# Performance work log

Hardware: AMD Instinct MI355X
Metric: run time of the kernel (lower is better)

Reference implementation:

```python
import jax, jax.numpy as jnp
import numpy as np

N, C, L = 1024, 3, 6000
CONV_CH = [20, 32, 64, 20]
K = 3            # conv kernel size, padding (K-1)//2 = 1 -> SAME
POOL = 2
HID = 100
FLAT_DIM = (L // POOL**4 + 2 * C + 1) * CONV_CH[-1]  # (375 + 7) * 20 = 7640


def setup_inputs() -> dict:
    key = jax.random.key(0)
    ks = jax.random.split(key, 10)
    d = {"x": jax.random.normal(ks[0], (N, C, L), jnp.float32)}
    ins = [C] + CONV_CH[:-1]
    for i, (ic, oc) in enumerate(zip(ins, CONV_CH)):
        d[f"w{i}"] = jax.random.normal(ks[1 + i], (oc, ic, K), jnp.float32) * (1.0 / np.sqrt(ic * K))
        d[f"b{i}"] = jnp.zeros((oc,), jnp.float32)
    d["wc"] = jax.random.normal(ks[6], (CONV_CH[-1], C, 1), jnp.float32) * (1.0 / np.sqrt(C))
    d["bc"] = jnp.zeros((CONV_CH[-1],), jnp.float32)
    d["wl0"] = jax.random.normal(ks[7], (HID, FLAT_DIM), jnp.float32) * (1.0 / np.sqrt(FLAT_DIM))
    d["bl0"] = jnp.zeros((HID,), jnp.float32)
    d["wl1"] = jax.random.normal(ks[8], (2, HID), jnp.float32) * (1.0 / np.sqrt(HID))
    d["bl1"] = jnp.zeros((2,), jnp.float32)
    return d


def conv1d(x, w, b, pad):
    # x: (N, C_in, L), w: (C_out, C_in, K)
    out = jax.lax.conv_general_dilated(x, w, (1,), [(pad, pad)],
                                       dimension_numbers=('NCH', 'OIH', 'NCH'))
    return out + b[None, :, None]


def maxpool2(x):
    n, c, l = x.shape  # l always even here (6000 / 2^k)
    return x.reshape(n, c, l // 2, 2).max(-1)


def cov_eig_feats(x):
    # batched covariance as a single contraction (avoids the O(N*L*C*C) bmm intermediate)
    n, c, l = x.shape
    diff = x - x.mean(-1, keepdims=True)
    cov = jnp.einsum('ncl,ndl->ncd', diff, diff) / (l - 1)  # (N, C, C)
    # cov is symmetric PSD -> eigh (real); torch uses generic eig and keeps real parts
    vals, vecs = jnp.linalg.eigh(cov)
    vals = vals[..., None] / vals.max()          # global max over batch, like torch
    cov = cov / jnp.abs(cov).max()
    return jnp.concatenate([cov, vals, vecs], axis=-1)  # (N, C, 2C+1)


def reference(x, w0, b0, w1, b1, w2, b2, w3, b3, wc, bc, wl0, bl0, wl1, bl1):
    feats = jax.lax.stop_gradient(cov_eig_feats(x))  # torch branch is @no_grad
    h = x
    for w, b in ((w0, b0), (w1, b1), (w2, b2), (w3, b3)):
        h = maxpool2(jax.nn.relu(conv1d(h, w, b, (K - 1) // 2)))
    h = h.reshape(h.shape[0], -1)                    # (N, 20*375)
    h1 = jax.nn.relu(conv1d(feats, wc, bc, 0))       # (N, 20, 7)
    h1 = h1.reshape(h1.shape[0], -1)
    h = jnp.concatenate([h, h1], axis=1)             # (N, 7640)
    h = jax.nn.relu(h @ wl0.T + bl0)
    out = h @ wl1.T + bl1                            # (N, 2)
    return (out[:, :1], out[:, 1:])
```

## Files before the change

### kernel.cpp

```cpp
#include <hip/hip_runtime.h>
#include <hip/hip_fp16.h>
#include <math.h>

#define NBATCH 1024
#define LIN    6000
#define HCATW  7640
#define HID    100

#define TCH   54
#define NCHK  7

#define ASZ 3552
#define BSZ 4460

#define W0OFF 0
#define W1OFF 192
#define W2OFF 2112
#define W3OFF 8256
#define B0OFF 12352
#define B1OFF 12372
#define B2OFF 12404
#define B3OFF 12468
#define WREPSZ 12496

#define WL0HSZ (HID * (HCATW/2))

#define FCNS 8

typedef _Float16 v2h __attribute__((ext_vector_type(2)));

__device__ __forceinline__ float fdot2_f16(unsigned int a, unsigned int b, float c) {
#if __has_builtin(__builtin_amdgcn_fdot2)
    v2h ah, bh;
    __builtin_memcpy(&ah, &a, 4);
    __builtin_memcpy(&bh, &b, 4);
    return __builtin_amdgcn_fdot2(ah, bh, c, false);
#else
    float d;
    asm("v_dot2_f32_f16 %0, %1, %2, %3" : "=v"(d) : "v"(a), "v"(b), "v"(c));
    return d;
#endif
}

__device__ __forceinline__ __half2 u2h2(unsigned int u) {
    __half2 h; __builtin_memcpy(&h, &u, 4); return h;
}

__device__ __forceinline__ void pack_pk16g(int idx, int OC, int IC, int OCG,
                                           int OPG, int WSTR,
                                           const float* __restrict__ w,
                                           unsigned int* __restrict__ dst)
{
    if (idx >= OCG * IC * WSTR) return;
    int ocg = idx / (IC * WSTR);
    int r   = idx - ocg * (IC * WSTR);
    int ic  = r / WSTR, q = r - ic * WSTR;
    int o   = q / 3, k = q - o * 3;
    int oc  = ocg * OPG + o;
    unsigned int v = 0;
    if (o < OPG && oc < OC) {
        float wv = w[(oc * IC + ic) * 3 + k];
        unsigned int h = __half_as_ushort(__float2half(wv));
        v = h | (h << 16);
    }
    dst[idx] = v;
}

__global__ __launch_bounds__(256) void prep_kernel(
    const float* __restrict__ w0, const float* __restrict__ b0,
    const float* __restrict__ w1, const float* __restrict__ b1,
    const float* __restrict__ w2, const float* __restrict__ b2,
    const float* __restrict__ w3, const float* __restrict__ b3,
    const float* __restrict__ wl0,
    float* __restrict__ wrep, unsigned int* __restrict__ wl0h)
{
    int idx = blockIdx.x * 256 + threadIdx.x;
    if (idx < WL0HSZ) {
        float a = wl0[idx * 2], b = wl0[idx * 2 + 1];
        unsigned int lo = __half_as_ushort(__float2half(a));
        unsigned int hi = __half_as_ushort(__float2half(b));
        wl0h[idx] = lo | (hi << 16);
    }
    if (idx < 8192) {
        unsigned int* wu = (unsigned int*)wrep;
        pack_pk16g(idx, 20,  3, 4, 5, 16, w0, wu + W0OFF);
        pack_pk16g(idx, 32, 20, 4, 8, 24, w1, wu + W1OFF);
        pack_pk16g(idx, 64, 32, 8, 8, 24, w2, wu + W2OFF);
        pack_pk16g(idx, 20, 64, 4, 5, 16, w3, wu + W3OFF);
        if (idx < 20)            wrep[B0OFF + idx] = b0[idx];
        else if (idx < 52)  { int i = idx - 20;  wrep[B1OFF + i] = b1[i]; }
        else if (idx < 116) { int i = idx - 52;  wrep[B2OFF + i] = b2[i]; }
        else if (idx < 136) { int i = idx - 116; wrep[B3OFF + i] = b3[i]; }
    }
}

template<int IC, int OC, int OCG, int OPG, int WSTR, int JOUT, int LG, int JBLK,
         bool FINAL>
__device__ __forceinline__ void stage_eo(const float* __restrict__ in,
                                         float* __restrict__ out,
                                         float* __restrict__ outg,
                                         const float* __restrict__ wrep,
                                         const float* __restrict__ brep,
                                         int pbase, int o3, int wv, int lane,
                                         int zero)
{
    constexpr int PIN  = JOUT + 1;
    constexpr int NJT  = (JOUT + 64 * JBLK - 1) / (64 * JBLK);
    for (int task = wv; task < OCG * NJT; task += 8) {
        const int ocg = task / NJT;
        const int jt  = task - ocg * NJT;
        const int j0  = jt * (64 * JBLK) + lane;
        const float* bp = brep + ocg * OPG;
        __half2 ap[JBLK][OPG];
#pragma unroll
        for (int t = 0; t < JBLK; ++t)
#pragma unroll
            for (int o = 0; o < OPG; ++o) {
                __half hb = __float2half(bp[o]);
                ap[t][o] = __halves2half2(hb, hb);
            }
        const float* wbase = wrep + ocg * (IC * WSTR) + zero;
#pragma unroll 1
        for (int ic = 0; ic < IC; ++ic) {
            const float* wp = wbase + ic * WSTR;
            float wr[WSTR];
#pragma unroll
            for (int q = 0; q < WSTR / 4; ++q)
                *(float4*)&wr[q * 4] = *(const float4*)(wp + q * 4);
#pragma unroll
            for (int t = 0; t < JBLK; ++t) {
                const int jj = j0 + t * 64;
                const int jc = (jj < JOUT) ? jj : (JOUT - 1);
                const float* ipw = in + ic * PIN;
                uint2 pw;
                __builtin_memcpy(&pw, ipw + jc, 8);
                const unsigned int crossu = (pw.x >> 16) | (pw.y << 16);
#pragma unroll
                for (int o = 0; o < OPG; ++o) {
                    __half2 a = ap[t][o];
                    a = __hfma2(u2h2(pw.x),   u2h2(__float_as_uint(wr[o*3+0])), a);
                    a = __hfma2(u2h2(crossu), u2h2(__float_as_uint(wr[o*3+1])), a);
                    a = __hfma2(u2h2(pw.y),   u2h2(__float_as_uint(wr[o*3+2])), a);
                    ap[t][o] = a;
                }
            }
        }

#pragma unroll
        for (int t = 0; t < JBLK; ++t) {
            const int jj = j0 + t * 64;
            if constexpr (FINAL) {
                const int gj = o3 + jj;
                if (gj < 375 && jj < JOUT) {
#pragma unroll
                    for (int o = 0; o < OPG; ++o) {
                        float ee = __low2float(ap[t][o]);
                        float oo = __high2float(ap[t][o]);
                        outg[(ocg*OPG+o) * 375 + gj] = fmaxf(fmaxf(ee, oo), 0.f);
                    }
                }
            } else {
                const int g = pbase + jj;
                const bool val = (jj < JOUT) && (g >= 0) && (g < LG);
                if (jj < JOUT) {
                    __half* dh = (__half*)out;
#pragma unroll
                    for (int o = 0; o < OPG; ++o) {
                        float ee = __low2float(ap[t][o]);
                        float oo = __high2float(ap[t][o]);
                        float v = val ? fmaxf(fmaxf(ee, oo), 0.f) : 0.f;
                        dh[(ocg*OPG+o) * JOUT + jj] = __float2half(v);
                    }
                }
            }
        }
    }
}

__device__ __forceinline__ void stage3_split(const float* __restrict__ in,
                                             float* __restrict__ part,
                                             float* __restrict__ outg,
                                             const float* __restrict__ wrep,
                                             const float* __restrict__ brep,
                                             int o3, int wv, int lane, int zero)
{
    constexpr int JOUT = 54, PIND = 55, OPG = 5, WSTR = 16;
    const int ocg = wv & 3, ih = wv >> 2;
    const int j  = lane;
    const int jc = (j < JOUT) ? j : (JOUT - 1);
    const float* bp = brep + ocg * OPG;
    __half2 ap[OPG];
#pragma unroll
    for (int o = 0; o < OPG; ++o) {
        __half hb = __float2half(ih ? 0.f : bp[o]);
        ap[o] = __halves2half2(hb, hb);
    }
    const float* wbase = wrep + (ocg * 64 + ih * 32) * WSTR + zero;
#pragma unroll 2
    for (int ic = 0; ic < 32; ++ic) {
        const float* ipw = in + (ih * 32 + ic) * PIND;
        uint2 pw;
        __builtin_memcpy(&pw, ipw + jc, 8);
        const unsigned int crossu = (pw.x >> 16) | (pw.y << 16);
        const float* wp = wbase + ic * WSTR;
        float wr[WSTR];
#pragma unroll
        for (int q = 0; q < WSTR / 4; ++q)
            *(float4*)&wr[q * 4] = *(const float4*)(wp + q * 4);
#pragma unroll
        for (int o = 0; o < OPG; ++o) {
            __half2 a = ap[o];
            a = __hfma2(u2h2(pw.x),   u2h2(__float_as_uint(wr[o*3+0])), a);
            a = __hfma2(u2h2(crossu), u2h2(__float_as_uint(wr[o*3+1])), a);
            a = __hfma2(u2h2(pw.y),   u2h2(__float_as_uint(wr[o*3+2])), a);
            ap[o] = a;
        }
    }
    unsigned int* pu = (unsigned int*)part;
    if (ih == 1) {
#pragma unroll
        for (int o = 0; o < OPG; ++o) {
            unsigned int u; __builtin_memcpy(&u, &ap[o], 4);
            pu[(ocg * OPG + o) * 64 + lane] = u;
        }
    }
    __syncthreads();
    if (ih == 0) {
        const int gj = o3 + j;
        if (gj < 375 && j < JOUT) {
#pragma unroll
            for (int o = 0; o < OPG; ++o) {
                __half2 p = u2h2(pu[(ocg * OPG + o) * 64 + lane]);
                float ee = __low2float(ap[o])  + __low2float(p);
                float oo = __high2float(ap[o]) + __high2float(p);
                outg[(ocg * OPG + o) * 375 + gj] = fmaxf(fmaxf(ee, oo), 0.f);
            }
        }
    }
}

__global__ __launch_bounds__(512, 8) void conv_chain_eo(
    const float* __restrict__ x,
    const float* __restrict__ wrep,
    float* __restrict__ hcat)
{
    __shared__ float A[ASZ];
    __shared__ float B[BSZ];

    const int tid  = threadIdx.x;
    const int wv   = __builtin_amdgcn_readfirstlane(tid >> 6);
    const int lane = tid & 63;
    const int zero = __builtin_amdgcn_ds_bpermute(0, 0);
    const int n     = blockIdx.x / NCHK;
    const int chunk = blockIdx.x % NCHK;
    const int o3 = chunk * TCH;
    const int p2 = 2*o3 - 1, p1 = 4*o3 - 3, p0 = 8*o3 - 7, xs = 16*o3 - 15;

    const float* xn = x + (size_t)n * 3 * LIN;
    unsigned int* Au = (unsigned int*)A;
    for (int idx = tid; idx < 3 * 447; idx += 512) {
        int c = idx / 447, p = idx - c * 447;
        int g0 = xs + 2 * p, g1 = g0 + 1;
        float v0 = (g0 >= 0 && g0 < LIN) ? xn[c * LIN + g0] : 0.f;
        float v1 = (g1 >= 0 && g1 < LIN) ? xn[c * LIN + g1] : 0.f;
        __half2 h = __floats2half2_rn(v0, v1);
        unsigned int u; __builtin_memcpy(&u, &h, 4);
        Au[c * 447 + p] = u;
    }
    __syncthreads();
    stage_eo< 3, 20, 4, 5, 16, 446, 3000, 2, false>(
        A, B, nullptr, wrep + W0OFF, wrep + B0OFF, p0, o3, wv, lane, zero);
    __syncthreads();
    stage_eo<20, 32, 4, 8, 24, 222, 1500, 2, false>(
        B, A, nullptr, wrep + W1OFF, wrep + B1OFF, p1, o3, wv, lane, zero);
    __syncthreads();
    stage_eo<32, 64, 8, 8, 24, 110,  750, 2, false>(
        A, B, nullptr, wrep + W2OFF, wrep + B2OFF, p2, o3, wv, lane, zero);
    __syncthreads();
    stage3_split(B, A, hcat + (size_t)n * HCATW,
                 wrep + W3OFF, wrep + B3OFF, o3, wv, lane, zero);
}

__device__ __forceinline__ float fsign(float a, float b) {
    return (b >= 0.0f) ? fabsf(a) : -fabsf(a);
}
__device__ __forceinline__ float slapy2(float xx, float yy) {
    float xa = fabsf(xx), ya = fabsf(yy);
    float w = fmaxf(xa, ya), z = fminf(xa, ya);
    if (z == 0.f) return w;
    float t = z / w;
    return w * sqrtf(1.f + t*t);
}
__device__ __forceinline__ void slartg(float f, float g, float& c, float& s, float& r) {
    if (g == 0.f)      { c = 1.f; s = 0.f; r = f; }
    else if (f == 0.f) { c = 0.f; s = (g >= 0.f ? 1.f : -1.f); r = fabsf(g); }
    else {
        float d = sqrtf(f*f + g*g);
        c = fabsf(f) / d;
        r = fsign(d, f);
        s = g / r;
    }
}
__device__ void slaev2(float a, float b, float cc,
                       float& rt1, float& rt2, float& cs1, float& sn1) {
    float sm = a + cc, df = a - cc;
    float adf = fabsf(df);
    float tb = b + b, ab = fabsf(tb);
    float acmx, acmn;
    if (fabsf(a) > fabsf(cc)) { acmx = a; acmn = cc; } else { acmx = cc; acmn = a; }
    float rt;
    if (adf > ab)      { float t = ab/adf; rt = adf*sqrtf(1.f + t*t); }
    else if (adf < ab) { float t = adf/ab; rt = ab*sqrtf(1.f + t*t); }
    else rt = ab * sqrtf(2.f);
    int sgn1;
    if (sm < 0.f)      { rt1 = 0.5f*(sm - rt); sgn1 = -1; rt2 = (acmx/rt1)*acmn - (b/rt1)*b; }
    else if (sm > 0.f) { rt1 = 0.5f*(sm + rt); sgn1 =  1; rt2 = (acmx/rt1)*acmn - (b/rt1)*b; }
    else               { rt1 = 0.5f*rt; rt2 = -0.5f*rt; sgn1 = 1; }
    float cs; int sgn2;
    if (df >= 0.f) { cs = df + rt; sgn2 = 1; } else { cs = df - rt; sgn2 = -1; }
    float acs = fabsf(cs);
    if (acs > ab) {
        float ct = -tb / cs;
        sn1 = 1.f / sqrtf(1.f + ct*ct);
        cs1 = ct * sn1;
    } else {
        if (ab == 0.f) { cs1 = 1.f; sn1 = 0.f; }
        else {
            float tn = -cs / tb;
            cs1 = 1.f / sqrtf(1.f + tn*tn);
            sn1 = tn * cs1;
        }
    }
    if (sgn1 == sgn2) { float tn = cs1; cs1 = -sn1; sn1 = tn; }
}
__device__ __forceinline__ void rot_cols(float z[3][3], int jc, float c, float s) {
    for (int i = 0; i < 3; ++i) {
        float t = z[i][jc+1];
        z[i][jc+1] = c*t - s*z[i][jc];
        z[i][jc]   = s*t + c*z[i][jc];
    }
}

__device__ void ssteqr3(float d[3], float e[2], float z[3][3]) {
    const float eps    = 5.9604645e-8f;
    const float eps2   = eps * eps;
    const float safmin = 1.17549435e-38f;
    const int n = 3;
    for (int i = 0; i < 3; ++i)
        for (int j = 0; j < 3; ++j) z[i][j] = (i == j) ? 1.f : 0.f;
    const int nmaxit = n * 30;
    int jtot = 0;
    float cw[2], sw[2];
    int l1 = 1, l, m, lend, lsv, lendsv;

L10:
    if (l1 > n) goto L160;
    if (l1 > 1) e[l1-2] = 0.f;
    if (l1 <= n-1) {
        for (m = l1; m <= n-1; ++m) {
            float tst = fabsf(e[m-1]);
            if (tst == 0.f) goto L30;
            if (tst <= (sqrtf(fabsf(d[m-1])) * sqrtf(fabsf(d[m]))) * eps) {
                e[m-1] = 0.f;
                goto L30;
            }
        }
    }
    m = n;
L30:
    l = l1; lsv = l; lend = m; lendsv = lend; l1 = m + 1;
    if (lend == l) goto L10;
    if (fabsf(d[lend-1]) < fabsf(d[l-1])) { lend = lsv; l = lendsv; }
    if (lend > l) {
L40:
        if (l != lend) {
            bool found = false;
            for (m = l; m <= lend-1; ++m) {
                float tst = e[m-1]*e[m-1];
                if (tst <= (eps2*fabsf(d[m-1]))*fabsf(d[m]) + safmin) { found = true; break; }
            }
            if (!found) m = lend;
        } else m = lend;
        if (m < lend) e[m-1] = 0.f;
        {
            float p = d[l-1];
            if (m == l) {
                d[l-1] = p;
                l = l + 1;
                if (l <= lend) goto L40;
                goto L140;
            }
            if (m == l+1) {
                float rt1, rt2, c2, s2;
                slaev2(d[l-1], e[l-1], d[l], rt1, rt2, c2, s2);
                rot_cols(z, l-1, c2, s2);
                d[l-1] = rt1; d[l] = rt2; e[l-1] = 0.f;
                l += 2;
                if (l <= lend) goto L40;
                goto L140;
            }
            if (jtot == nmaxit) goto L140;
            jtot++;
            float g = (d[l] - p) / (2.f * e[l-1]);
            float r = slapy2(g, 1.f);
            g = d[m-1] - p + e[l-1] / (g + fsign(r, g));
            float s = 1.f, c = 1.f;
            p = 0.f;
            for (int i = m-1; i >= l; --i) {
                float f = s * e[i-1];
                float b = c * e[i-1];
                slartg(g, f, c, s, r);
                if (i != m-1) e[i] = r;
                g = d[i] - p;
                r = (d[i-1] - g)*s + 2.f*c*b;
                p = s * r;
                d[i] = g + p;
                g = c*r - b;
                cw[i-l] = c; sw[i-l] = -s;
            }
            for (int jj = m-l; jj >= 1; --jj)
                rot_cols(z, l + jj - 2, cw[jj-1], sw[jj-1]);
            d[l-1] = d[l-1] - p;
            e[l-1] = g;
            goto L40;
        }
    } else {
L90:
        if (l != lend) {
            bool found = false;
            for (m = l; m >= lend+1; --m) {
                float tst = e[m-2]*e[m-2];
                if (tst <= (eps2*fabsf(d[m-1]))*fabsf(d[m-2]) + safmin) { found = true; break; }
            }
            if (!found) m = lend;
        } else m = lend;
        if (m > lend) e[m-2] = 0.f;
        {
            float p = d[l-1];
            if (m == l) {
                d[l-1] = p;
                l = l - 1;
                if (l >= lend) goto L90;
                goto L140;
            }
            if (m == l-1) {
                float rt1, rt2, c2, s2;
                slaev2(d[l-2], e[l-2], d[l-1], rt1, rt2, c2, s2);
                rot_cols(z, l-2, c2, s2);
                d[l-2] = rt1; d[l-1] = rt2; e[l-2] = 0.f;
                l -= 2;
                if (l >= lend) goto L90;
                goto L140;
            }
            if (jtot == nmaxit) goto L140;
            jtot++;
            float g = (d[l-2] - p) / (2.f * e[l-2]);
            float r = slapy2(g, 1.f);
            g = d[m-1] - p + e[l-2] / (g + fsign(r, g));
            float s = 1.f, c = 1.f;
            p = 0.f;
            for (int i = m; i <= l-1; ++i) {
                float f = s * e[i-1];
                float b = c * e[i-1];
                slartg(g, f, c, s, r);
                if (i != m) e[i-2] = r;
                g = d[i-1] - p;
                r = (d[i] - g)*s + 2.f*c*b;
                p = s * r;
                d[i-1] = g + p;
                g = c*r - b;
                cw[i-m] = c; sw[i-m] = s;
            }
            for (int jj = 1; jj <= l-m; ++jj)
                rot_cols(z, m + jj - 2, cw[jj-1], sw[jj-1]);
            d[l-1] = d[l-1] - p;
            e[l-2] = g;
            goto L90;
        }
    }
L140:
    if (jtot < nmaxit) goto L10;
L160:
    for (int ii = 2; ii <= n; ++ii) {
        int i = ii - 1, k = i;
        float p = d[i-1];
        for (int j = ii; j <= n; ++j)
            if (d[j-1] < p) { k = j; p = d[j-1]; }
        if (k != i) {
            d[k-1] = d[i-1]; d[i-1] = p;
            for (int r0 = 0; r0 < 3; ++r0) {
                float t = z[r0][i-1]; z[r0][i-1] = z[r0][k-1]; z[r0][k-1] = t;
            }
        }
    }
}

__global__ __launch_bounds__(256) void cov_eig_kernel(const float* __restrict__ x,
                                                      float* __restrict__ eigbuf,
                                                      unsigned int* __restrict__ gmax)
{
    __shared__ float part[4][9];
    const int n = blockIdx.x;
    const float* xn = x + (size_t)n * 3 * LIN;
    float v[9] = {0,0,0,0,0,0,0,0,0};
    for (int i = threadIdx.x; i < LIN / 4; i += 256) {
        float4 a = *(const float4*)(xn + 4 * i);
        float4 b = *(const float4*)(xn + LIN + 4 * i);
        float4 c = *(const float4*)(xn + 2 * LIN + 4 * i);
        v[0] += (a.x + a.y) + (a.z + a.w);
        v[1] += (b.x + b.y) + (b.z + b.w);
        v[2] += (c.x + c.y) + (c.z + c.w);
        v[3] = fmaf(a.x,a.x, fmaf(a.y,a.y, fmaf(a.z,a.z, fmaf(a.w,a.w, v[3]))));
        v[4] = fmaf(a.x,b.x, fmaf(a.y,b.y, fmaf(a.z,b.z, fmaf(a.w,b.w, v[4]))));
        v[5] = fmaf(a.x,c.x, fmaf(a.y,c.y, fmaf(a.z,c.z, fmaf(a.w,c.w, v[5]))));
        v[6] = fmaf(b.x,b.x, fmaf(b.y,b.y, fmaf(b.z,b.z, fmaf(b.w,b.w, v[6]))));
        v[7] = fmaf(b.x,c.x, fmaf(b.y,c.y, fmaf(b.z,c.z, fmaf(b.w,c.w, v[7]))));
        v[8] = fmaf(c.x,c.x, fmaf(c.y,c.y, fmaf(c.z,c.z, fmaf(c.w,c.w, v[8]))));
    }
#pragma unroll
    for (int off = 32; off > 0; off >>= 1)
#pragma unroll
        for (int i = 0; i < 9; ++i) v[i] += __shfl_down(v[i], off, 64);
    const int wv = threadIdx.x >> 6, lane = threadIdx.x & 63;
    if (lane == 0)
        for (int i = 0; i < 9; ++i) part[wv][i] = v[i];
    __syncthreads();
    if (threadIdx.x == 0) {
        float t[9];
        for (int i = 0; i < 9; ++i)
            t[i] = part[0][i] + part[1][i] + part[2][i] + part[3][i];
        const float Lf = (float)LIN;
        float m0 = t[0]/Lf, m1 = t[1]/Lf, m2 = t[2]/Lf;
        float c00 = (t[3] - Lf*m0*m0) / (Lf - 1.f);
        float c01 = (t[4] - Lf*m0*m1) / (Lf - 1.f);
        float c02 = (t[5] - Lf*m0*m2) / (Lf - 1.f);
        float c11 = (t[6] - Lf*m1*m1) / (Lf - 1.f);
        float c12 = (t[7] - Lf*m1*m2) / (Lf - 1.f);
        float c22 = (t[8] - Lf*m2*m2) / (Lf - 1.f);

        float dd[3], ee[2], tau, v2;
        {
            float a21 = c01, a31 = c02, a22 = c11, a32 = c12, a33 = c22;
            float xnorm = fabsf(a31);
            if (xnorm == 0.f) {
                tau = 0.f; v2 = 0.f;
                dd[0] = c00; dd[1] = a22; dd[2] = a33;
                ee[0] = a21; ee[1] = a32;
            } else {
                float beta = -fsign(slapy2(a21, xnorm), a21);
                tau = (beta - a21) / beta;
                v2  = a31 / (a21 - beta);
                ee[0] = beta;
                float x1 = tau*(a22 + a32*v2);
                float x2 = tau*(a32 + a33*v2);
                float al = -0.5f*tau*(x1 + x2*v2);
                float w1 = x1 + al;
                float w2 = x2 + al*v2;
                a22 -= 2.f*w1;
                a32 -= (v2*w1 + w2);
                a33 -= 2.f*v2*w2;
                dd[0] = c00; dd[1] = a22; dd[2] = a33;
                ee[1] = a32;
            }
        }
        float zz[3][3];
        ssteqr3(dd, ee, zz);
        if (tau != 0.f) {
            for (int j = 0; j < 3; ++j) {
                float sum = zz[1][j] + v2*zz[2][j];
                zz[1][j] -= tau * sum;
                zz[2][j] -= tau * v2 * sum;
            }
        }

        float* eb = eigbuf + n * 21;
        eb[0] = c00; eb[1] = c01; eb[2] = c02;
        eb[3] = c01; eb[4] = c11; eb[5] = c12;
        eb[6] = c02; eb[7] = c12; eb[8] = c22;
        eb[9] = dd[0]; eb[10] = dd[1]; eb[11] = dd[2];
        for (int c = 0; c < 3; ++c)
            for (int k = 0; k < 3; ++k) eb[12 + c*3 + k] = zz[c][k];

        float vmax = fmaxf(dd[0], fmaxf(dd[1], dd[2]));
        float cmax = 0.f;
        for (int i = 0; i < 9; ++i) cmax = fmaxf(cmax, fabsf(eb[i]));
        atomicMax(&gmax[0], __float_as_uint(vmax));
        atomicMax(&gmax[1], __float_as_uint(cmax));
    }
}

__global__ __launch_bounds__(256) void feats_kernel(const float* __restrict__ eigbuf,
                                                    const unsigned int* __restrict__ gmax,
                                                    const float* __restrict__ wc,
                                                    const float* __restrict__ bc,
                                                    float* __restrict__ hcat)
{
    const int n = blockIdx.x;
    const int t = threadIdx.x;
    if (t >= 140) return;
    const int o = t / 7, j = t % 7;
    const float* eb = eigbuf + n * 21;
    const float vmax = __uint_as_float(gmax[0]);
    const float cmax = __uint_as_float(gmax[1]);
    float f0, f1, f2;
    if (j < 3)       { f0 = eb[0*3+j]/cmax; f1 = eb[1*3+j]/cmax; f2 = eb[2*3+j]/cmax; }
    else if (j == 3) { f0 = eb[9]/vmax;     f1 = eb[10]/vmax;    f2 = eb[11]/vmax; }
    else             { int k = j-4; f0 = eb[12+0*3+k]; f1 = eb[12+1*3+k]; f2 = eb[12+2*3+k]; }
    float r = bc[o] + wc[o*3+0]*f0 + wc[o*3+1]*f1 + wc[o*3+2]*f2;
    hcat[(size_t)n*HCATW + 7500 + o*7 + j] = fmaxf(r, 0.f);
}

__global__ __launch_bounds__(512) void fc01_kernel(const float* __restrict__ hcat,
                                                   const unsigned int* __restrict__ wl0h,
                                                   const float* __restrict__ bl0,
                                                   const float* __restrict__ wl1,
                                                   const float* __restrict__ bl1,
                                                   float* __restrict__ out)
{
    __shared__ __half hl[FCNS * HCATW];
    __shared__ float hbuf[FCNS * HID];
    const int tid = threadIdx.x;
    const int n0 = blockIdx.x * FCNS;
    for (int i = tid; i < FCNS * (HCATW/4); i += 512) {
        int s  = i / (HCATW/4);
        int k4 = i - s * (HCATW/4);
        float4 v = *(const float4*)(hcat + (size_t)(n0 + s) * HCATW + k4 * 4);
        __half2 h01 = __floats2half2_rn(v.x, v.y);
        __half2 h23 = __floats2half2_rn(v.z, v.w);
        *(__half2*)(hl + s * HCATW + k4 * 4)     = h01;
        *(__half2*)(hl + s * HCATW + k4 * 4 + 2) = h23;
    }
    __syncthreads();
    const int wv = tid >> 6;
    const int lane = tid & 63;
    for (int ot = wv; ot < HID / 4; ot += 8) {
        float acc[4][FCNS];
#pragma unroll
        for (int oo = 0; oo < 4; ++oo)
#pragma unroll
            for (int s = 0; s < FCNS; ++s) acc[oo][s] = 0.f;
        for (int k = lane * 8; k < HCATW; k += 512) {
            uint4 hv[FCNS];
#pragma unroll
            for (int s = 0; s < FCNS; ++s)
                hv[s] = *(const uint4*)(hl + s * HCATW + k);
#pragma unroll
            for (int oo = 0; oo < 4; ++oo) {
                const uint4 wp = *(const uint4*)(wl0h + (ot*4+oo) * (HCATW/2) + (k >> 1));
#pragma unroll
                for (int s = 0; s < FCNS; ++s) {
                    float a = acc[oo][s];
                    a = fdot2_f16(hv[s].x, wp.x, a);
                    a = fdot2_f16(hv[s].y, wp.y, a);
                    a = fdot2_f16(hv[s].z, wp.z, a);
                    a = fdot2_f16(hv[s].w, wp.w, a);
                    acc[oo][s] = a;
                }
            }
        }
#pragma unroll
        for (int off = 32; off > 0; off >>= 1)
#pragma unroll
            for (int oo = 0; oo < 4; ++oo)
#pragma unroll
                for (int s = 0; s < FCNS; ++s)
                    acc[oo][s] += __shfl_down(acc[oo][s], off, 64);
        if (lane == 0) {
#pragma unroll
            for (int oo = 0; oo < 4; ++oo) {
                const float b = bl0[ot*4+oo];
#pragma unroll
                for (int s = 0; s < FCNS; ++s)
                    hbuf[s * HID + ot*4+oo] = fmaxf(acc[oo][s] + b, 0.f);
            }
        }
    }
    __syncthreads();
    if (tid < 2 * FCNS) {
        const int s = tid >> 1, r = tid & 1;
        const float* w = wl1 + r * HID;
        float acc = bl1[r];
        for (int k = 0; k < HID; ++k) acc = fmaf(hbuf[s * HID + k], w[k], acc);
        out[r * NBATCH + n0 + s] = acc;
    }
}

extern "C" void kernel_launch(void* const* d_in, const int* in_sizes, int n_in,
                              void* d_out, int out_size, void* d_ws, size_t ws_size,
                              hipStream_t stream)
{
    const float* x   = (const float*)d_in[0];
    const float* w0  = (const float*)d_in[1];
    const float* b0  = (const float*)d_in[2];
    const float* w1  = (const float*)d_in[3];
    const float* b1  = (const float*)d_in[4];
    const float* w2  = (const float*)d_in[5];
    const float* b2  = (const float*)d_in[6];
    const float* w3  = (const float*)d_in[7];
    const float* b3  = (const float*)d_in[8];
    const float* wc  = (const float*)d_in[9];
    const float* bc  = (const float*)d_in[10];
    const float* wl0 = (const float*)d_in[11];
    const float* bl0 = (const float*)d_in[12];
    const float* wl1 = (const float*)d_in[13];
    const float* bl1 = (const float*)d_in[14];
    float* out = (float*)d_out;

    const size_t HCAT_N = (size_t)NBATCH * HCATW;
    const size_t EIG_N  = (size_t)NBATCH * 21;
    const size_t need_bytes = (HCAT_N + EIG_N + 4 + WREPSZ + WL0HSZ) * 4 + 16;
    if (ws_size < need_bytes) return;

    float* ws     = (float*)d_ws;
    float* hcat   = ws;
    float* eigbuf = hcat + HCAT_N;
    unsigned int* gmax = (unsigned int*)(eigbuf + EIG_N);
    float* wrep   = (float*)(gmax + 4);
    unsigned int* wl0h = (unsigned int*)(wrep + WREPSZ);

    hipMemsetAsync(gmax, 0, 2 * sizeof(unsigned int), stream);

    prep_kernel<<<(WL0HSZ + 255) / 256, 256, 0, stream>>>(
        w0, b0, w1, b1, w2, b2, w3, b3, wl0, wrep, wl0h);
    conv_chain_eo<<<NBATCH * NCHK, 512, 0, stream>>>(x, wrep, hcat);
    cov_eig_kernel<<<NBATCH, 256, 0, stream>>>(x, eigbuf, gmax);
    feats_kernel<<<NBATCH, 256, 0, stream>>>(eigbuf, gmax, wc, bc, hcat);
    fc01_kernel<<<NBATCH / FCNS, 512, 0, stream>>>(hcat, wl0h, bl0, wl1, bl1, out);
}
```

Before: 605.8 us.

## Store hcat as fp16 and split FC0 reduction over K into two blocks

The conv chain and feature kernels now write the concatenated activation buffer in half precision, which halves its global write and read traffic and removes the float-to-half conversion in the FC kernel. FC0 is split along the reduction dimension into two halves, doubling the grid from 128 to 256 blocks and shrinking per-block shared memory. Each half writes fp32 partial sums to a new buffer, and a separate fc1 kernel adds the partials, bias and ReLU and applies the final layer. This costs an extra launch and a partial-sum round trip through global memory.

```diff
diff --git a/kernel.cpp b/kernel.cpp
--- a/kernel.cpp
+++ b/kernel.cpp
@@ -26,6 +26,7 @@
 #define WL0HSZ (HID * (HCATW/2))
 
 #define FCNS 8
+#define KSPL 3824
 
 typedef _Float16 v2h __attribute__((ext_vector_type(2)));
 
@@ -98,7 +99,7 @@
          bool FINAL>
 __device__ __forceinline__ void stage_eo(const float* __restrict__ in,
                                          float* __restrict__ out,
-                                         float* __restrict__ outg,
+                                         __half* __restrict__ outg,
                                          const float* __restrict__ wrep,
                                          const float* __restrict__ brep,
                                          int pbase, int o3, int wv, int lane,
@@ -156,7 +157,8 @@
                     for (int o = 0; o < OPG; ++o) {
                         float ee = __low2float(ap[t][o]);
                         float oo = __high2float(ap[t][o]);
-                        outg[(ocg*OPG+o) * 375 + gj] = fmaxf(fmaxf(ee, oo), 0.f);
+                        outg[(ocg*OPG+o) * 375 + gj] =
+                            __float2half(fmaxf(fmaxf(ee, oo), 0.f));
                     }
                 }
             } else {
@@ -179,7 +181,7 @@
 
 __device__ __forceinline__ void stage3_split(const float* __restrict__ in,
                                              float* __restrict__ part,
-                                             float* __restrict__ outg,
+                                             __half* __restrict__ outg,
                                              const float* __restrict__ wrep,
                                              const float* __restrict__ brep,
                                              int o3, int wv, int lane, int zero)
@@ -233,7 +235,8 @@
                 __half2 p = u2h2(pu[(ocg * OPG + o) * 64 + lane]);
                 float ee = __low2float(ap[o])  + __low2float(p);
                 float oo = __high2float(ap[o]) + __high2float(p);
-                outg[(ocg * OPG + o) * 375 + gj] = fmaxf(fmaxf(ee, oo), 0.f);
+                outg[(ocg * OPG + o) * 375 + gj] =
+                    __float2half(fmaxf(fmaxf(ee, oo), 0.f));
             }
         }
     }
@@ -242,7 +245,7 @@
 __global__ __launch_bounds__(512, 8) void conv_chain_eo(
     const float* __restrict__ x,
     const float* __restrict__ wrep,
-    float* __restrict__ hcat)
+    __half* __restrict__ hcat)
 {
     __shared__ float A[ASZ];
     __shared__ float B[BSZ];
@@ -593,7 +596,7 @@
                                                     const unsigned int* __restrict__ gmax,
                                                     const float* __restrict__ wc,
                                                     const float* __restrict__ bc,
-                                                    float* __restrict__ hcat)
+                                                    __half* __restrict__ hcat)
 {
     const int n = blockIdx.x;
     const int t = threadIdx.x;
@@ -607,28 +610,25 @@
     else if (j == 3) { f0 = eb[9]/vmax;     f1 = eb[10]/vmax;    f2 = eb[11]/vmax; }
     else             { int k = j-4; f0 = eb[12+0*3+k]; f1 = eb[12+1*3+k]; f2 = eb[12+2*3+k]; }
     float r = bc[o] + wc[o*3+0]*f0 + wc[o*3+1]*f1 + wc[o*3+2]*f2;
-    hcat[(size_t)n*HCATW + 7500 + o*7 + j] = fmaxf(r, 0.f);
-}
-
-__global__ __launch_bounds__(512) void fc01_kernel(const float* __restrict__ hcat,
-                                                   const unsigned int* __restrict__ wl0h,
-                                                   const float* __restrict__ bl0,
-                                                   const float* __restrict__ wl1,
-                                                   const float* __restrict__ bl1,
-                                                   float* __restrict__ out)
-{
-    __shared__ __half hl[FCNS * HCATW];
-    __shared__ float hbuf[FCNS * HID];
+    hcat[(size_t)n*HCATW + 7500 + o*7 + j] = __float2half(fmaxf(r, 0.f));
+}
+
+__global__ __launch_bounds__(512) void fc0_kernel(const __half* __restrict__ hcat,
+                                                  const unsigned int* __restrict__ wl0h,
+                                                  float* __restrict__ hpart)
+{
+    __shared__ __half hl[FCNS * KSPL];
     const int tid = threadIdx.x;
-    const int n0 = blockIdx.x * FCNS;
-    for (int i = tid; i < FCNS * (HCATW/4); i += 512) {
-        int s  = i / (HCATW/4);
-        int k4 = i - s * (HCATW/4);
-        float4 v = *(const float4*)(hcat + (size_t)(n0 + s) * HCATW + k4 * 4);
-        __half2 h01 = __floats2half2_rn(v.x, v.y);
-        __half2 h23 = __floats2half2_rn(v.z, v.w);
-        *(__half2*)(hl + s * HCATW + k4 * 4)     = h01;
-        *(__half2*)(hl + s * HCATW + k4 * 4 + 2) = h23;
+    const int g  = blockIdx.x >> 1;
+    const int kh = blockIdx.x & 1;
+    const int k0   = kh ? KSPL : 0;
+    const int KLEN = kh ? (HCATW - KSPL) : KSPL;
+    const int n0 = g * FCNS;
+    for (int i = tid; i < FCNS * (KLEN / 8); i += 512) {
+        int s  = i / (KLEN / 8);
+        int k8 = i - s * (KLEN / 8);
+        *(uint4*)(hl + s * KLEN + k8 * 8) =
+            *(const uint4*)(hcat + (size_t)(n0 + s) * HCATW + k0 + k8 * 8);
     }
     __syncthreads();
     const int wv = tid >> 6;
@@ -639,14 +639,15 @@
         for (int oo = 0; oo < 4; ++oo)
 #pragma unroll
             for (int s = 0; s < FCNS; ++s) acc[oo][s] = 0.f;
-        for (int k = lane * 8; k < HCATW; k += 512) {
+        for (int k = lane * 8; k < KLEN; k += 512) {
             uint4 hv[FCNS];
 #pragma unroll
             for (int s = 0; s < FCNS; ++s)
-                hv[s] = *(const uint4*)(hl + s * HCATW + k);
+                hv[s] = *(const uint4*)(hl + s * KLEN + k);
 #pragma unroll
             for (int oo = 0; oo < 4; ++oo) {
-                const uint4 wp = *(const uint4*)(wl0h + (ot*4+oo) * (HCATW/2) + (k >> 1));
+                const uint4 wp = *(const uint4*)(wl0h + (ot*4+oo) * (HCATW/2)
+                                                 + ((k0 + k) >> 1));
 #pragma unroll
                 for (int s = 0; s < FCNS; ++s) {
                     float a = acc[oo][s];
@@ -667,22 +668,33 @@
                     acc[oo][s] += __shfl_down(acc[oo][s], off, 64);
         if (lane == 0) {
 #pragma unroll
-            for (int oo = 0; oo < 4; ++oo) {
-                const float b = bl0[ot*4+oo];
+            for (int oo = 0; oo < 4; ++oo)
 #pragma unroll
                 for (int s = 0; s < FCNS; ++s)
-                    hbuf[s * HID + ot*4+oo] = fmaxf(acc[oo][s] + b, 0.f);
-            }
-        }
-    }
-    __syncthreads();
-    if (tid < 2 * FCNS) {
-        const int s = tid >> 1, r = tid & 1;
-        const float* w = wl1 + r * HID;
-        float acc = bl1[r];
-        for (int k = 0; k < HID; ++k) acc = fmaf(hbuf[s * HID + k], w[k], acc);
-        out[r * NBATCH + n0 + s] = acc;
-    }
+                    hpart[((size_t)kh * NBATCH + n0 + s) * HID + ot*4+oo] =
+                        acc[oo][s];
+        }
+    }
+}
+
+__global__ __launch_bounds__(256) void fc1_kernel(const float* __restrict__ hpart,
+                                                  const float* __restrict__ bl0,
+                                                  const float* __restrict__ wl1,
+                                                  const float* __restrict__ bl1,
+                                                  float* __restrict__ out)
+{
+    int idx = blockIdx.x * 256 + threadIdx.x;
+    if (idx >= 2 * NBATCH) return;
+    const int s = idx >> 1, r = idx & 1;
+    const float* p0 = hpart + (size_t)s * HID;
+    const float* p1 = hpart + ((size_t)NBATCH + s) * HID;
+    const float* w = wl1 + r * HID;
+    float acc = bl1[r];
+    for (int k = 0; k < HID; ++k) {
+        float h = fmaxf(p0[k] + p1[k] + bl0[k], 0.f);
+        acc = fmaf(h, w[k], acc);
+    }
+    out[r * NBATCH + s] = acc;
 }
 
 extern "C" void kernel_launch(void* const* d_in, const int* in_sizes, int n_in,
@@ -708,15 +720,17 @@
 
     const size_t HCAT_N = (size_t)NBATCH * HCATW;
     const size_t EIG_N  = (size_t)NBATCH * 21;
-    const size_t need_bytes = (HCAT_N + EIG_N + 4 + WREPSZ + WL0HSZ) * 4 + 16;
+    const size_t HPART_N = 2 * (size_t)NBATCH * HID;
+    const size_t need_bytes = HCAT_N * 2 +
+        (EIG_N + 4 + WREPSZ + WL0HSZ + HPART_N) * 4 + 16;
     if (ws_size < need_bytes) return;
 
-    float* ws     = (float*)d_ws;
-    float* hcat   = ws;
-    float* eigbuf = hcat + HCAT_N;
+    __half* hcat  = (__half*)d_ws;
+    float* eigbuf = (float*)(hcat + HCAT_N);
     unsigned int* gmax = (unsigned int*)(eigbuf + EIG_N);
     float* wrep   = (float*)(gmax + 4);
     unsigned int* wl0h = (unsigned int*)(wrep + WREPSZ);
+    float* hpart  = (float*)(wl0h + WL0HSZ);
 
     hipMemsetAsync(gmax, 0, 2 * sizeof(unsigned int), stream);
 
@@ -725,5 +739,6 @@
     conv_chain_eo<<<NBATCH * NCHK, 512, 0, stream>>>(x, wrep, hcat);
     cov_eig_kernel<<<NBATCH, 256, 0, stream>>>(x, eigbuf, gmax);
     feats_kernel<<<NBATCH, 256, 0, stream>>>(eigbuf, gmax, wc, bc, hcat);
-    fc01_kernel<<<NBATCH / FCNS, 512, 0, stream>>>(hcat, wl0h, bl0, wl1, bl1, out);
-}
+    fc0_kernel<<<(NBATCH / FCNS) * 2, 512, 0, stream>>>(hcat, wl0h, hpart);
+    fc1_kernel<<<(2 * NBATCH + 255) / 256, 256, 0, stream>>>(hpart, bl0, wl1, bl1, out);
+}
```

Measured after the change: 595.4 us. Within noise of the previous version (-1.7%).
